# Kernel optimization log

Hardware: AMD Instinct MI355X
Metric: run time of the kernel (lower is better)

Reference implementation:

```python
import jax, jax.numpy as jnp
import numpy as np

V = 100000   # vocab_size
D = 128      # d_model
N = 262144   # number of (target, context) training pairs
K = 5        # num_negatives


def setup_inputs() -> dict:
    key = jax.random.key(0)
    k1, k2, k3, k4, k5 = jax.random.split(key, 5)
    emb = jax.random.normal(k1, (V, D), dtype=jnp.float32)      # input embedding table
    out_w = jax.random.normal(k2, (V, D), dtype=jnp.float32)    # output (Linear) weight [V, D]
    tgt_ids = jax.random.randint(k3, (N,), 0, V)
    ctx_ids = jax.random.randint(k4, (N,), 0, V)
    neg_ids = jax.random.randint(k5, (N, K), 0, V)
    return {"emb": emb, "out_w": out_w, "tgt_ids": tgt_ids,
            "ctx_ids": ctx_ids, "neg_ids": neg_ids}


def reference(emb, out_w, tgt_ids, ctx_ids, neg_ids):
    # Batched skip-gram with negative sampling (SGNS), faithful to the
    # per-pair math in _train_skipgram:
    #   input_e = embeddings(tgt); pos_e = weight.weight[ctx]
    #   neg_e   = weight.weight[neg_ids]
    #   loss    = -(logsigmoid(<input_e, pos_e>) + sum logsigmoid(-neg_e @ input_e))
    input_e = emb[tgt_ids]            # [N, D]
    pos_e = out_w[ctx_ids]            # [N, D]
    neg_e = out_w[neg_ids]            # [N, K, D]

    pos_score = jnp.sum(input_e * pos_e, axis=-1)            # [N]
    neg_score = jnp.einsum('nkd,nd->nk', neg_e, input_e)     # [N, K]

    loss = -(jax.nn.log_sigmoid(pos_score)
             + jnp.sum(jax.nn.log_sigmoid(-neg_score), axis=-1))  # [N]
    return loss
```

## Files before the change

kernel.cpp:

```cpp
#include <hip/hip_runtime.h>
#include <hip/hip_fp16.h>
#include <math.h>


#define D 128
#define K 5

typedef _Float16 h2 __attribute__((ext_vector_type(2)));

__device__ __forceinline__ float log_sigmoid(float x) {
    return fminf(x, 0.0f) - __logf(1.0f + __expf(-fabsf(x)));
}

__device__ __forceinline__ float dot8_f16(uint4 a, uint4 b, float acc) {
    acc = __builtin_amdgcn_fdot2(__builtin_bit_cast(h2, a.x),
                                 __builtin_bit_cast(h2, b.x), acc, false);
    acc = __builtin_amdgcn_fdot2(__builtin_bit_cast(h2, a.y),
                                 __builtin_bit_cast(h2, b.y), acc, false);
    acc = __builtin_amdgcn_fdot2(__builtin_bit_cast(h2, a.z),
                                 __builtin_bit_cast(h2, b.z), acc, false);
    acc = __builtin_amdgcn_fdot2(__builtin_bit_cast(h2, a.w),
                                 __builtin_bit_cast(h2, b.w), acc, false);
    return acc;
}

__device__ __forceinline__ void gload16(const void* gptr, void* lptr) {
    __builtin_amdgcn_global_load_lds(
        (const __attribute__((address_space(1))) void*)gptr,
        (__attribute__((address_space(3))) void*)lptr,
        16, 0, 0);
}

struct H8 { __half2 a, b, c, d; };

__global__ __launch_bounds__(256) void cvt2_f16_kernel(
    const float* __restrict__ src0, const float* __restrict__ src1,
    __half* __restrict__ dst0, __half* __restrict__ dst1, int n )
{
    int i = (blockIdx.x * blockDim.x + threadIdx.x) * 8;
    const float* src = src0;
    __half* dst = dst0;
    if (i >= n) { src = src1; dst = dst1; i -= n; }
    if (i >= n) return;
    float4 x = *(const float4*)(src + i);
    float4 y = *(const float4*)(src + i + 4);
    H8 h;
    h.a = __floats2half2_rn(x.x, x.y);
    h.b = __floats2half2_rn(x.z, x.w);
    h.c = __floats2half2_rn(y.x, y.y);
    h.d = __floats2half2_rn(y.z, y.w);
    *(H8*)(dst + i) = h;
}

__global__ __launch_bounds__(256) void sgns_f16_lds_kernel(
    const __half* __restrict__ embh,
    const __half* __restrict__ outh,
    const int* __restrict__ tgt_ids,
    const int* __restrict__ ctx_ids,
    const int* __restrict__ neg_ids,
    float* __restrict__ out,
    int N)
{
    __shared__ alignas(16) char smem[4 * 7 * 1024];

    const int lane = threadIdx.x & 63;
    const int wave = threadIdx.x >> 6;
    const int lg   = lane & 15;
    const int grp  = lane >> 4;
    const int n_raw = (blockIdx.x * 4 + wave) * 4 + grp;
    const bool valid = n_raw < N;
    const int n = valid ? n_raw : N - 1;

    const int t = tgt_ids[n];
    int rows[K + 1];
    rows[0] = ctx_ids[n];
    {
        const int4 n4 = *(const int4*)(neg_ids + (size_t)n * K);
        rows[1] = n4.x; rows[2] = n4.y; rows[3] = n4.z; rows[4] = n4.w;
        rows[5] = neg_ids[(size_t)n * K + 4];
    }

    char* wbase = smem + wave * (7 * 1024);

    gload16(embh + (size_t)t * D + lg * 8, wbase);
#pragma unroll
    for (int j = 0; j < K + 1; ++j)
        gload16(outh + (size_t)rows[j] * D + lg * 8,
                wbase + (j + 1) * 1024);

    asm volatile("s_waitcnt vmcnt(0)" ::: "memory");
#if __has_builtin(__builtin_amdgcn_sched_barrier)
    __builtin_amdgcn_sched_barrier(0);
#endif

    const char* myfrag = wbase + lane * 16;
    const uint4 in = *(const uint4*)(myfrag);
    float dot[K + 1];
#pragma unroll
    for (int j = 0; j < K + 1; ++j) {
        const uint4 w = *(const uint4*)(myfrag + (j + 1) * 1024);
        dot[j] = dot8_f16(in, w, 0.0f);
    }

#pragma unroll
    for (int j = 0; j < K + 1; ++j) {
        float v = dot[j];
        v += __shfl_xor(v, 1);
        v += __shfl_xor(v, 2);
        v += __shfl_xor(v, 4);
        v += __shfl_xor(v, 8);
        dot[j] = v;
    }

    if (lg == 0 && valid) {
        float loss = log_sigmoid(dot[0]);
#pragma unroll
        for (int j = 1; j < K + 1; ++j)
            loss += log_sigmoid(-dot[j]);
        out[n] = -loss;
    }
}

__global__ __launch_bounds__(256) void sgns_f32_kernel(
    const float* __restrict__ emb,
    const float* __restrict__ out_w,
    const int* __restrict__ tgt_ids,
    const int* __restrict__ ctx_ids,
    const int* __restrict__ neg_ids,
    float* __restrict__ out,
    int N)
{
    const int lane = threadIdx.x & 63;
    const int wave = threadIdx.x >> 6;
    const int lg   = lane & 15;
    const int grp  = lane >> 4;
    const int n = (blockIdx.x * 4 + wave) * 4 + grp;
    if (n >= N) return;

    const int t = tgt_ids[n];
    int rows[K + 1];
    rows[0] = ctx_ids[n];
    const int4 n4 = *(const int4*)(neg_ids + (size_t)n * K);
    rows[1] = n4.x; rows[2] = n4.y; rows[3] = n4.z; rows[4] = n4.w;
    rows[5] = neg_ids[(size_t)n * K + 4];

    const float4* er = (const float4*)(emb + (size_t)t * D);
    const float4 in0 = er[lg];
    const float4 in1 = er[lg + 16];

    float4 w0[K + 1], w1[K + 1];
#pragma unroll
    for (int j = 0; j < K + 1; ++j) {
        const float4* wr = (const float4*)(out_w + (size_t)rows[j] * D);
        w0[j] = wr[lg];
        w1[j] = wr[lg + 16];
    }

    float dot[K + 1];
#pragma unroll
    for (int j = 0; j < K + 1; ++j) {
        dot[j] = in0.x * w0[j].x + in0.y * w0[j].y
               + in0.z * w0[j].z + in0.w * w0[j].w
               + in1.x * w1[j].x + in1.y * w1[j].y
               + in1.z * w1[j].z + in1.w * w1[j].w;
    }

#pragma unroll
    for (int j = 0; j < K + 1; ++j) {
        float v = dot[j];
        v += __shfl_xor(v, 1);
        v += __shfl_xor(v, 2);
        v += __shfl_xor(v, 4);
        v += __shfl_xor(v, 8);
        dot[j] = v;
    }

    if (lg == 0) {
        float loss = log_sigmoid(dot[0]);
#pragma unroll
        for (int j = 1; j < K + 1; ++j)
            loss += log_sigmoid(-dot[j]);
        out[n] = -loss;
    }
}

extern "C" void kernel_launch(void* const* d_in, const int* in_sizes, int n_in,
                              void* d_out, int out_size, void* d_ws, size_t ws_size,
                              hipStream_t stream) {
    const float* emb     = (const float*)d_in[0];
    const float* out_w   = (const float*)d_in[1];
    const int*   tgt_ids = (const int*)d_in[2];
    const int*   ctx_ids = (const int*)d_in[3];
    const int*   neg_ids = (const int*)d_in[4];
    float* out = (float*)d_out;

    const int N = in_sizes[2];
    const size_t vd = (size_t)in_sizes[0];
    const size_t need = 2 * vd * sizeof(__half);

    if (ws_size >= need) {
        __half* embh = (__half*)d_ws;
        __half* outh = embh + vd;
        const int cvt_threads = (int)(2 * vd / 8);
        const int cvt_blocks = (cvt_threads + 255) / 256;
        cvt2_f16_kernel<<<cvt_blocks, 256, 0, stream>>>(emb, out_w, embh, outh,
                                                        (int)vd);
        const int blocks = (N + 15) / 16;
        sgns_f16_lds_kernel<<<blocks, 256, 0, stream>>>(embh, outh, tgt_ids,
                                                        ctx_ids, neg_ids, out, N);
    } else {
        const int blocks = (N + 15) / 16;
        sgns_f32_kernel<<<blocks, 256, 0, stream>>>(emb, out_w, tgt_ids,
                                                    ctx_ids, neg_ids, out, N);
    }
}
```

Baseline: 190.5 us.

## Pipeline gathers with double-buffered LDS in persistent single-wave blocks

Replaces the one-shot gather kernel with a persistent grid of single-wave blocks. Each wave loops over sets of four pairs, prefetching the next set's indices and issuing its async global-to-LDS row loads into a second buffer while computing the current set. A partial vmcnt wait lets the next set's loads stay in flight during compute. This aims to hide gather latency with explicit software pipelining rather than relying on occupancy, but it drops the N%4 tail handling and depends on the hand-counted vmcnt value being correct.

```diff
diff --git a/kernel.cpp b/kernel.cpp
--- a/kernel.cpp
+++ b/kernel.cpp
@@ -52,7 +52,26 @@
     *(H8*)(dst + i) = h;
 }
 
-__global__ __launch_bounds__(256) void sgns_f16_lds_kernel(
+#define LOAD_IDX(set, t, r)                                                  \
+    do {                                                                     \
+        const int _n = (set) * 4 + grp;                                      \
+        (t) = tgt_ids[_n];                                                   \
+        (r)[0] = ctx_ids[_n];                                                \
+        const int4 _n4 = *(const int4*)(neg_ids + (size_t)_n * K);           \
+        (r)[1] = _n4.x; (r)[2] = _n4.y; (r)[3] = _n4.z; (r)[4] = _n4.w;      \
+        (r)[5] = neg_ids[(size_t)_n * K + 4];                                \
+    } while (0)
+
+#define ISSUE(t, r, buf)                                                     \
+    do {                                                                     \
+        gload16(embh + (size_t)(t) * D + lg * 8, (buf));                     \
+        _Pragma("unroll")                                                    \
+        for (int _j = 0; _j < K + 1; ++_j)                                   \
+            gload16(outh + (size_t)(r)[_j] * D + lg * 8,                     \
+                    (char*)(buf) + (_j + 1) * 1024);                         \
+    } while (0)
+
+__global__ __launch_bounds__(64) void sgns_f16_pipe_kernel(
     const __half* __restrict__ embh,
     const __half* __restrict__ outh,
     const int* __restrict__ tgt_ids,
@@ -61,63 +80,76 @@
     float* __restrict__ out,
     int N)
 {
-    __shared__ alignas(16) char smem[4 * 7 * 1024];
+    __shared__ alignas(16) char smem[2][7 * 1024];
 
     const int lane = threadIdx.x & 63;
-    const int wave = threadIdx.x >> 6;
     const int lg   = lane & 15;
     const int grp  = lane >> 4;
-    const int n_raw = (blockIdx.x * 4 + wave) * 4 + grp;
-    const bool valid = n_raw < N;
-    const int n = valid ? n_raw : N - 1;
-
-    const int t = tgt_ids[n];
-    int rows[K + 1];
-    rows[0] = ctx_ids[n];
+    const int total  = N >> 2;
+    const int stride = gridDim.x;
+    int s = blockIdx.x;
+    if (s >= total) return;
+
+    int t_c, r_c[K + 1];
+    int t_n, r_n[K + 1];
+    LOAD_IDX(s, t_c, r_c);
     {
-        const int4 n4 = *(const int4*)(neg_ids + (size_t)n * K);
-        rows[1] = n4.x; rows[2] = n4.y; rows[3] = n4.z; rows[4] = n4.w;
-        rows[5] = neg_ids[(size_t)n * K + 4];
-    }
-
-    char* wbase = smem + wave * (7 * 1024);
-
-    gload16(embh + (size_t)t * D + lg * 8, wbase);
-#pragma unroll
-    for (int j = 0; j < K + 1; ++j)
-        gload16(outh + (size_t)rows[j] * D + lg * 8,
-                wbase + (j + 1) * 1024);
-
-    asm volatile("s_waitcnt vmcnt(0)" ::: "memory");
+        int s1 = s + stride; if (s1 >= total) s1 = total - 1;
+        LOAD_IDX(s1, t_n, r_n);
+    }
+    ISSUE(t_c, r_c, smem[0]);
+    int cur = 0;
+
+    for (;;) {
+        const int next = s + stride;
+        const bool last = next >= total;
+        if (!last) {
+            int s2 = next + stride; if (s2 >= total) s2 = total - 1;
+            int t_nn, r_nn[K + 1];
+            LOAD_IDX(s2, t_nn, r_nn);
 #if __has_builtin(__builtin_amdgcn_sched_barrier)
-    __builtin_amdgcn_sched_barrier(0);
+            __builtin_amdgcn_sched_barrier(0);
 #endif
-
-    const char* myfrag = wbase + lane * 16;
-    const uint4 in = *(const uint4*)(myfrag);
-    float dot[K + 1];
-#pragma unroll
-    for (int j = 0; j < K + 1; ++j) {
-        const uint4 w = *(const uint4*)(myfrag + (j + 1) * 1024);
-        dot[j] = dot8_f16(in, w, 0.0f);
-    }
-
-#pragma unroll
-    for (int j = 0; j < K + 1; ++j) {
-        float v = dot[j];
-        v += __shfl_xor(v, 1);
-        v += __shfl_xor(v, 2);
-        v += __shfl_xor(v, 4);
-        v += __shfl_xor(v, 8);
-        dot[j] = v;
-    }
-
-    if (lg == 0 && valid) {
-        float loss = log_sigmoid(dot[0]);
-#pragma unroll
-        for (int j = 1; j < K + 1; ++j)
-            loss += log_sigmoid(-dot[j]);
-        out[n] = -loss;
+            ISSUE(t_n, r_n, smem[cur ^ 1]);
+            t_n = t_nn;
+#pragma unroll
+            for (int j = 0; j < K + 1; ++j) r_n[j] = r_nn[j];
+            asm volatile("s_waitcnt vmcnt(11)" ::: "memory");
+        } else {
+            asm volatile("s_waitcnt vmcnt(0)" ::: "memory");
+        }
+#if __has_builtin(__builtin_amdgcn_sched_barrier)
+        __builtin_amdgcn_sched_barrier(0);
+#endif
+
+        const char* myfrag = (const char*)smem[cur] + lane * 16;
+        const uint4 in = *(const uint4*)myfrag;
+        float dot[K + 1];
+#pragma unroll
+        for (int j = 0; j < K + 1; ++j) {
+            const uint4 w = *(const uint4*)(myfrag + (j + 1) * 1024);
+            dot[j] = dot8_f16(in, w, 0.0f);
+        }
+#pragma unroll
+        for (int j = 0; j < K + 1; ++j) {
+            float v = dot[j];
+            v += __shfl_xor(v, 1);
+            v += __shfl_xor(v, 2);
+            v += __shfl_xor(v, 4);
+            v += __shfl_xor(v, 8);
+            dot[j] = v;
+        }
+        if (lg == 0) {
+            float loss = log_sigmoid(dot[0]);
+#pragma unroll
+            for (int j = 1; j < K + 1; ++j)
+                loss += log_sigmoid(-dot[j]);
+            out[s * 4 + grp] = -loss;
+        }
+
+        if (last) break;
+        s = next;
+        cur ^= 1;
     }
 }
 
@@ -205,8 +237,10 @@
         const int cvt_blocks = (cvt_threads + 255) / 256;
         cvt2_f16_kernel<<<cvt_blocks, 256, 0, stream>>>(emb, out_w, embh, outh,
                                                         (int)vd);
-        const int blocks = (N + 15) / 16;
-        sgns_f16_lds_kernel<<<blocks, 256, 0, stream>>>(embh, outh, tgt_ids,
+        const int total_sets = N / 4;
+        int blocks = 256 * 11;
+        if (blocks > total_sets) blocks = total_sets;
+        sgns_f16_pipe_kernel<<<blocks, 64, 0, stream>>>(embh, outh, tgt_ids,
                                                         ctx_ids, neg_ids, out, N);
     } else {
         const int blocks = (N + 15) / 16;
```

After: 220.5 us. 15.7% more time.
